# Kernel optimization log

Hardware: AMD Instinct MI355X
Metric: run time of the kernel (lower is better)

Reference implementation:

```python
import math
import jax, jax.numpy as jnp
import numpy as np

# ---------------- static irrep configuration ----------------
RS_IN = [(16, 0, 0), (16, 1, 0)]
RS_OUT = [(16, 0, 0), (16, 1, 0)]


def selection_rule(l_in, p_in, l_out, p_out):
    return [l for l in range(abs(l_in - l_out), l_in + l_out + 1)
            if p_out == 0 or p_in * (-1) ** l == p_out]


# ---------------- real Wigner 3j (Clebsch-Gordan) ----------------

def _su2_cg(j1, j2, j3, m1, m2, m3):
    if m1 + m2 != m3:
        return 0.0
    f = math.factorial
    pref = math.sqrt((2 * j3 + 1) * f(j3 + j1 - j2) * f(j3 - j1 + j2) * f(j1 + j2 - j3) / f(j1 + j2 + j3 + 1))
    pref *= math.sqrt(f(j3 + m3) * f(j3 - m3) * f(j1 - m1) * f(j1 + m1) * f(j2 - m2) * f(j2 + m2))
    s = 0.0
    for k in range(0, j1 + j2 - j3 + 1):
        d = [k, j1 + j2 - j3 - k, j1 - m1 - k, j2 + m2 - k, j3 - j1 - m2 + k, j3 - j2 + m1 + k]
        if any(x < 0 for x in d):
            continue
        s += (-1) ** k / np.prod([float(f(x)) for x in d])
    return pref * s


def _c2r(l):
    # real SH = A @ complex SH, rows/cols ordered m = -l..l
    A = np.zeros((2 * l + 1, 2 * l + 1), dtype=complex)
    s2 = 1.0 / math.sqrt(2)
    for m in range(-l, l + 1):
        if m < 0:
            A[l + m, l + m] = 1j * s2
            A[l + m, l - m] = -1j * (-1) ** m * s2
        elif m == 0:
            A[l, l] = 1.0
        else:
            A[l + m, l - m] = s2
            A[l + m, l + m] = (-1) ** m * s2
    return A


_W3J_CACHE = {}

def wigner_3j(l1, l2, l3):
    key = (l1, l2, l3)
    if key in _W3J_CACHE:
        return _W3J_CACHE[key]
    C = np.zeros((2 * l1 + 1, 2 * l2 + 1, 2 * l3 + 1))
    for m1 in range(-l1, l1 + 1):
        for m2 in range(-l2, l2 + 1):
            m3 = -(m1 + m2)
            if abs(m3) <= l3:
                C[l1 + m1, l2 + m2, l3 + m3] = ((-1) ** (l1 - l2 - m3) / math.sqrt(2 * l3 + 1)
                                                * _su2_cg(l1, l2, l3, m1, m2, -m3))
    T = np.einsum('ia,jb,kc,abc->ijk', _c2r(l1), _c2r(l2), _c2r(l3), C.astype(complex))
    T = T * (-1j) ** (l1 + l2 + l3)
    re, im = np.real(T), np.imag(T)
    T = re if np.abs(re).sum() >= np.abs(im).sum() else im
    n = math.sqrt(float((T ** 2).sum()))
    T = T / n if n > 1e-12 else T
    _W3J_CACHE[key] = T
    return T


# ---------------- real spherical harmonics (l = 0,1,2) ----------------

def real_sh(ls, xyz):
    r = jnp.linalg.norm(xyz, axis=-1)
    n = xyz / jnp.where(r > 0, r, 1.0)[..., None]
    x, y, z = n[..., 0], n[..., 1], n[..., 2]
    out = []
    for l in ls:
        if l == 0:
            out.append(jnp.full(x.shape, 0.28209479177387814, x.dtype)[None])
        elif l == 1:
            c = 0.4886025119029199
            out.append(jnp.stack([c * y, c * z, c * x]))
        elif l == 2:
            c1 = 1.0925484305920792
            c2 = 0.31539156525252005
            c3 = 0.5462742152960396
            out.append(jnp.stack([c1 * x * y, c1 * y * z, c2 * (3 * z * z - 1), c1 * x * z, c3 * (x * x - y * y)]))
        else:
            raise NotImplementedError
    return jnp.concatenate(out, axis=0)  # [sum(2l+1), batch, a, b]


def _norm_coef_table():
    nc = np.zeros((len(RS_OUT), len(RS_IN), 2))
    for i, (mul_out, l_out, p_out) in enumerate(RS_OUT):
        num = sum(mul_in * len(selection_rule(l_in, p_in, l_out, p_out))
                  for (mul_in, l_in, p_in) in RS_IN)
        for j, (mul_in, l_in, p_in) in enumerate(RS_IN):
            lm = math.sqrt(2 * l_in + 1) * math.sqrt(4 * math.pi)
            nc[i, j, 0] = lm / math.sqrt(num)
            nc[i, j, 1] = lm / math.sqrt(mul_in)
    return nc


def kernel_conv(features, geometry, mask, W1, b1, W2, b2):
    batch, a, b, _ = geometry.shape
    set_of_l_filters = sorted({l for (_, li, pi) in RS_IN for (_, lo, po) in RS_OUT
                               for l in selection_rule(li, pi, lo, po)})
    Y = real_sh(set_of_l_filters, geometry)             # [9, z, a, b]
    radii = jnp.linalg.norm(geometry, axis=-1)          # [z, a, b]
    # radial MLP: 1 -> H -> n_path
    h = jax.nn.relu(radii[..., None] * W1[0] + b1)
    R = h @ W2 + b2                                     # [z, a, b, n_path]
    nc = _norm_coef_table()
    is_zero = radii == 0

    out_blocks = []
    begin_R = 0
    for i, (mul_out, l_out, p_out) in enumerate(RS_OUT):
        block = jnp.zeros((batch, a, mul_out, 2 * l_out + 1), features.dtype)
        begin_in = 0
        for j, (mul_in, l_in, p_in) in enumerate(RS_IN):
            s_in = slice(begin_in, begin_in + mul_in * (2 * l_in + 1))
            begin_in += mul_in * (2 * l_in + 1)
            l_filters = selection_rule(l_in, p_in, l_out, p_out)
            if not l_filters:
                continue
            n = mul_out * mul_in * len(l_filters)
            sub_R = R[..., begin_R:begin_R + n].reshape(batch, a, b, mul_out, mul_in, len(l_filters))
            begin_R += n
            sub_nc = jnp.where(is_zero, nc[i, j, 1], nc[i, j, 0]).astype(features.dtype)
            f_in = features[..., s_in].reshape(batch, b, mul_in, 2 * l_in + 1)
            for k, l_f in enumerate(l_filters):
                offset = sum(2 * l + 1 for l in set_of_l_filters if l < l_f)
                sub_Y = Y[offset:offset + 2 * l_f + 1]
                C = jnp.asarray(wigner_3j(l_out, l_in, l_f), features.dtype)
                block = block + jnp.einsum('ijk,kzab,zabuv,zab,zbvj->zaui',
                                           C, sub_Y, sub_R[..., k], sub_nc, f_in)
        out_blocks.append(block.reshape(batch, a, -1))
    out = jnp.concatenate(out_blocks, axis=-1)          # [z, a, n_out]
    return out * mask[..., None]


def setup_inputs() -> dict:
    key = jax.random.key(0)
    ks = jax.random.split(key, 6)
    batch, a, b = 2, 160, 160
    dim_in, n_path, H = 64, 1536, 64
    return {
        'features': jax.random.normal(ks[0], (batch, b, dim_in), jnp.float32),
        'geometry': jax.random.normal(ks[1], (batch, a, b, 3), jnp.float32),
        'mask': jnp.ones((batch, b), jnp.float32),
        'W1': jax.random.normal(ks[2], (1, H), jnp.float32) * 0.5,
        'b1': jax.random.normal(ks[3], (H,), jnp.float32) * 0.1,
        'W2': jax.random.normal(ks[4], (H, n_path), jnp.float32) / np.sqrt(H),
        'b2': jnp.zeros((n_path,), jnp.float32),
    }


def reference(features, geometry, mask, W1, b1, W2, b2):
    return kernel_conv(features, geometry, mask, W1, b1, W2, b2)
```

## Files before the change

kernel.cpp:

```cpp
#include <hip/hip_runtime.h>
#include <hip/hip_fp16.h>
#include <math.h>

#define NPATH 1536
#define NSEG  65
#define NB    160
#define NA    160
#define CW    32
#define PPW   5

__device__ float  dg_thr[64];
__device__ float4 dg_tbl4[NSEG * 512];

static __device__ __forceinline__ __half2 bc_h2(float x) {
    union { float f; __half2 h; } u; u.f = x; return u.h;
}
static __device__ __forceinline__ unsigned short h_us(__half h) {
    union { __half h; unsigned short s; } u; u.h = h; return u.s;
}

__global__ __launch_bounds__(256) void k_prep(const float* __restrict__ W1,
                                              const float* __restrict__ b1,
                                              const float* __restrict__ W2,
                                              const float* __restrict__ b2,
                                              float* __restrict__ out) {
    int bid = blockIdx.x, tid = threadIdx.x;
    if (bid >= 390) {
        out[(bid - 390) * 256 + tid] = 0.0f;
        return;
    }
    int tseg = bid / 6, tcol = bid % 6;
    __shared__ float tv[64], mw[64], mb[64];
    if (tid < 64) {
        float w = W1[tid], b = b1[tid];
        tv[tid] = (w != 0.0f) ? (-b / w) : __builtin_inff();
    }
    __syncthreads();
    if (tid < 64) {
        float mine = tv[tid];
        int rank = 0;
        for (int j = 0; j < 64; ++j) {
            float o = tv[j];
            rank += (o < mine || (o == mine && j < tid)) ? 1 : 0;
        }
        float w = W1[tid], b = b1[tid];
        bool act = (w > 0.0f) ? (rank < tseg)
                 : (w < 0.0f) ? (rank >= tseg)
                              : (b > 0.0f);
        mw[tid] = act ? w : 0.0f;
        mb[tid] = act ? b : 0.0f;
        if (bid == 0) dg_thr[tid] = mine;
    }
    __syncthreads();

    int p = tcol * 256 + tid;
    int e, k; float scl;
    if (p < 768) {
        int u = (p >> 4) & 15, v = p & 15, vu = v * 16 + u;
        if (p < 256)      { e = vu;       k = 0; scl = 0.17677669529663687f; }
        else if (p < 512) { e = vu;       k = 1; scl = 0.6266570686577502f;  }
        else              { e = 256 + vu; k = 0; scl = 0.2558286876965162f;  }
    } else {
        int m = (p - 768) / 3, kk = (p - 768) % 3;
        int u = m >> 4, v = m & 15, vu = v * 16 + u;
        e = 256 + vu;
        if (kk == 0)      { k = 1; scl = 0.125f;              }
        else if (kk == 1) { k = 2; scl = 0.3133285343288751f; }
        else              { k = 3; scl = 0.7674950309598664f; }
    }

    float A = 0.0f, B = 0.0f;
    #pragma unroll 8
    for (int c = 0; c < 64; ++c) {
        float w2 = W2[c * NPATH + p];
        A = fmaf(mw[c], w2, A);
        B = fmaf(mb[c], w2, B);
    }
    float sv = scl * A;
    float iv = scl * (B + b2[p]);

    unsigned short* ub = (unsigned short*)dg_tbl4 + ((size_t)tseg * 512 + e) * 8;
    ub[k]     = h_us(__float2half(sv));
    ub[4 + k] = h_us(__float2half(iv));
    if (p < 256) {
        ((unsigned int*)ub)[1] = 0u;
        ((unsigned int*)ub)[3] = 0u;
    }
}

__global__ __launch_bounds__(256, 4) void k_main(const float* __restrict__ feat,
                                                 const float* __restrict__ geom,
                                                 const float* __restrict__ mask,
                                                 float* __restrict__ out) {
    int wv   = threadIdx.x >> 6;
    int lane = threadIdx.x & 63;
    int gw   = blockIdx.x * 4 + wv;
    int chunk = gw & (CW - 1);
    int za    = gw >> 5;
    int z     = za / NA;

    __shared__ __align__(16) float sFeat[4][PPW][64];
    __shared__ float sAcc[4][64];

    const bool is0 = lane < 16;
    int u  = is0 ? lane : ((lane - 16) / 3);
    int i3 = is0 ? 0 : ((lane - 16) % 3);
    int waddr = is0 ? (lane * 4 + 3) : (((lane - 16) / 3) * 4 + ((lane - 16) % 3));

    int o_base = (is0 ? 0 : 256) + u;
    float zfl  = is0 ? 1.4142135623730951f : 2.0f;
    float bx = (!is0 && i3 == 0) ? 1.0f : 0.0f;
    float by = (!is0 && i3 == 1) ? 1.0f : 0.0f;
    float bz = (!is0 && i3 == 2) ? 1.0f : 0.0f;

    float thrv = dg_thr[lane];

    const float is30 = 0.18257418583505536f;
    const float is10 = 0.31622776601683794f;
    const float c1sh = 0.4886025119029199f;
    const float c21 = 1.0925484305920792f, c22 = 0.31539156525252005f, c23 = 0.5462742152960396f;

    int b0 = chunk * PPW;
    #pragma unroll
    for (int it = 0; it < PPW; ++it) {
        float fv = feat[((size_t)(z * NB + b0 + it)) * 64 + lane];
        sFeat[wv][it][waddr] = fv;
    }

    float rr[PPW], nxa[PPW], nya[PPW], nza[PPW], zfa[PPW];
    int rowo[PPW];
    #pragma unroll
    for (int it = 0; it < PPW; ++it) {
        const float* g = geom + ((size_t)za * NB + b0 + it) * 3;
        float gx = g[0], gy = g[1], gz = g[2];
        float r = sqrtf(gx * gx + gy * gy + gz * gz);
        bool zr = (r == 0.0f);
        float inv = zr ? 1.0f : (1.0f / r);
        nxa[it] = gx * inv; nya[it] = gy * inv; nza[it] = gz * inv;
        rr[it] = r;
        zfa[it] = zr ? zfl : 1.0f;
        unsigned long long bm = __ballot(thrv < r);
        rowo[it] = __popcll(bm) * 512;
    }

    float acc = 0.0f;

    #pragma unroll
    for (int it = 0; it < PPW; ++it) {
        float r = rr[it];

        const float4* __restrict__ rowp = dg_tbl4 + rowo[it] + o_base;
        const float*  sp = &sFeat[wv][it][0];
        float T0 = 0.0f;
        float T1x = 0.0f, T1y = 0.0f, T1z = 0.0f;
        float T2x = 0.0f, T2y = 0.0f, T2z = 0.0f;
        float T3x = 0.0f, T3y = 0.0f, T3z = 0.0f;
        #pragma unroll
        for (int v = 0; v < 16; ++v) {
            float4 t = rowp[v * 16];
            __half2 hs01 = bc_h2(t.x), hs23 = bc_h2(t.y);
            __half2 hi01 = bc_h2(t.z), hi23 = bc_h2(t.w);
            float R0 = fmaf(r, __low2float(hs01),  __low2float(hi01));
            float R1 = fmaf(r, __high2float(hs01), __high2float(hi01));
            float R2 = fmaf(r, __low2float(hs23),  __low2float(hi23));
            float R3 = fmaf(r, __high2float(hs23), __high2float(hi23));
            float4 fq = *(const float4*)&sp[4 * v];
            T0  = fmaf(R0, fq.w, T0);
            T1x = fmaf(R1, fq.x, T1x);
            T1y = fmaf(R1, fq.y, T1y);
            T1z = fmaf(R1, fq.z, T1z);
            T2x = fmaf(R2, fq.x, T2x);
            T2y = fmaf(R2, fq.y, T2y);
            T2z = fmaf(R2, fq.z, T2z);
            T3x = fmaf(R3, fq.x, T3x);
            T3y = fmaf(R3, fq.y, T3y);
            T3z = fmaf(R3, fq.z, T3z);
        }

        float nx = nxa[it], ny = nya[it], nz = nza[it];
        float Y1_0 = c1sh * ny, Y1_1 = c1sh * nz, Y1_2 = c1sh * nx;
        float Y2_0 = c21 * nx * ny;
        float Y2_1 = c21 * ny * nz;
        float Y2_2 = c22 * fmaf(3.0f, nz * nz, -1.0f);
        float Y2_3 = c21 * nx * nz;
        float Y2_4 = c23 * (nx * nx - ny * ny);

        float Yi = (i3 == 0) ? Y1_0 : (i3 == 1) ? Y1_1 : Y1_2;
        float c0 = is0 ? 1.0f : Yi;
        float d1x = is0 ? Y1_0 : bx;
        float d1y = is0 ? Y1_1 : by;
        float d1z = is0 ? Y1_2 : bz;
        float d2x = (i3 == 0) ? 0.0f   : (i3 == 1) ? -Y1_2 : Y1_1;
        float d2y = (i3 == 0) ? Y1_2   : (i3 == 1) ? 0.0f  : -Y1_0;
        float d2z = (i3 == 0) ? -Y1_1  : (i3 == 1) ? Y1_0  : 0.0f;
        float za_ = is10 * Y2_0, zb_ = is10 * Y2_1, zc_ = is10 * Y2_3;
        float zd_ = is30 * Y2_2, ze_ = is10 * Y2_4;
        float d3x = (i3 == 0) ? (-zd_ - ze_) : (i3 == 1) ? zb_ : za_;
        float d3y = (i3 == 0) ? zb_ : (i3 == 1) ? (2.0f * zd_) : zc_;
        float d3z = (i3 == 0) ? za_ : (i3 == 1) ? zc_ : (ze_ - zd_);

        float s = c0 * T0;
        s = fmaf(d1x, T1x, s); s = fmaf(d1y, T1y, s); s = fmaf(d1z, T1z, s);
        s = fmaf(d2x, T2x, s); s = fmaf(d2y, T2y, s); s = fmaf(d2z, T2z, s);
        s = fmaf(d3x, T3x, s); s = fmaf(d3y, T3y, s); s = fmaf(d3z, T3z, s);
        acc = fmaf(s, zfa[it], acc);
    }

    sAcc[wv][lane] = acc;
    __syncthreads();
    if (threadIdx.x < 64) {
        float sum = sAcc[0][threadIdx.x] + sAcc[1][threadIdx.x]
                  + sAcc[2][threadIdx.x] + sAcc[3][threadIdx.x];
        sum *= mask[za];
        atomicAdd(&out[(size_t)za * 64 + threadIdx.x], sum);
    }
}

extern "C" void kernel_launch(void* const* d_in, const int* in_sizes, int n_in,
                              void* d_out, int out_size, void* d_ws, size_t ws_size,
                              hipStream_t stream) {
    (void)in_sizes; (void)n_in; (void)d_ws; (void)ws_size; (void)out_size;
    const float* feat = (const float*)d_in[0];
    const float* geom = (const float*)d_in[1];
    const float* mask = (const float*)d_in[2];
    const float* W1   = (const float*)d_in[3];
    const float* b1   = (const float*)d_in[4];
    const float* W2   = (const float*)d_in[5];
    const float* b2   = (const float*)d_in[6];
    float* out = (float*)d_out;

    k_prep<<<470, 256, 0, stream>>>(W1, b1, W2, b2, out);
    k_main<<<2 * NA * CW / 4, 256, 0, stream>>>(feat, geom, mask, out);
}
```

Before: 104.8 us.

## Split v-reduction across wave halves and recombine with cross-lane shuffles

```diff
diff --git a/kernel.cpp b/kernel.cpp
--- a/kernel.cpp
+++ b/kernel.cpp
@@ -102,16 +102,25 @@
     __shared__ __align__(16) float sFeat[4][PPW][64];
     __shared__ float sAcc[4][64];
 
-    const bool is0 = lane < 16;
-    int u  = is0 ? lane : ((lane - 16) / 3);
-    int i3 = is0 ? 0 : ((lane - 16) % 3);
-    int waddr = is0 ? (lane * 4 + 3) : (((lane - 16) / 3) * 4 + ((lane - 16) % 3));
-
-    int o_base = (is0 ? 0 : 256) + u;
-    float zfl  = is0 ? 1.4142135623730951f : 2.0f;
-    float bx = (!is0 && i3 == 0) ? 1.0f : 0.0f;
-    float by = (!is0 && i3 == 1) ? 1.0f : 0.0f;
-    float bz = (!is0 && i3 == 2) ? 1.0f : 0.0f;
+    int h    = lane >> 5;
+    int l32  = lane & 31;
+    bool tl0 = l32 < 16;
+    int  tu  = l32 & 15;
+    int  e_base = (tl0 ? 0 : 256) + h * 16 + tu;
+
+    bool is0o = lane < 16;
+    int  grp  = lane >> 4;
+    int  i3o  = (grp == 2) ? 2 : (grp == 3) ? 1 : 0;
+    int  uo   = lane & 15;
+    int  outI = is0o ? uo : (16 + uo * 3 + i3o);
+    bool useSw = (grp == 2);
+    float zfl = is0o ? 1.4142135623730951f : 2.0f;
+    float bx = (i3o == 0) ? 1.0f : 0.0f;
+    float by = (i3o == 1) ? 1.0f : 0.0f;
+    float bz = (i3o == 2) ? 1.0f : 0.0f;
+
+    int waddr = (lane < 16) ? (lane * 4 + 3)
+                            : (((lane - 16) / 3) * 4 + ((lane - 16) % 3));
 
     float thrv = dg_thr[lane];
 
@@ -149,22 +158,22 @@
     for (int it = 0; it < PPW; ++it) {
         float r = rr[it];
 
-        const float4* __restrict__ rowp = dg_tbl4 + rowo[it] + o_base;
-        const float*  sp = &sFeat[wv][it][0];
+        const float4* __restrict__ rowp = dg_tbl4 + rowo[it] + e_base;
+        const float*  spL = &sFeat[wv][it][0] + h * 4;
         float T0 = 0.0f;
         float T1x = 0.0f, T1y = 0.0f, T1z = 0.0f;
         float T2x = 0.0f, T2y = 0.0f, T2z = 0.0f;
         float T3x = 0.0f, T3y = 0.0f, T3z = 0.0f;
         #pragma unroll
-        for (int v = 0; v < 16; ++v) {
-            float4 t = rowp[v * 16];
+        for (int s = 0; s < 8; ++s) {
+            float4 t = rowp[s * 32];
             __half2 hs01 = bc_h2(t.x), hs23 = bc_h2(t.y);
             __half2 hi01 = bc_h2(t.z), hi23 = bc_h2(t.w);
             float R0 = fmaf(r, __low2float(hs01),  __low2float(hi01));
             float R1 = fmaf(r, __high2float(hs01), __high2float(hi01));
             float R2 = fmaf(r, __low2float(hs23),  __low2float(hi23));
             float R3 = fmaf(r, __high2float(hs23), __high2float(hi23));
-            float4 fq = *(const float4*)&sp[4 * v];
+            float4 fq = *(const float4*)&spL[s * 8];
             T0  = fmaf(R0, fq.w, T0);
             T1x = fmaf(R1, fq.x, T1x);
             T1y = fmaf(R1, fq.y, T1y);
@@ -177,6 +186,13 @@
             T3z = fmaf(R3, fq.z, T3z);
         }
 
+        #define COMB(t) { t += __shfl_xor(t, 32); float _w = __shfl_xor(t, 48); t = useSw ? _w : t; }
+        COMB(T0)
+        COMB(T1x) COMB(T1y) COMB(T1z)
+        COMB(T2x) COMB(T2y) COMB(T2z)
+        COMB(T3x) COMB(T3y) COMB(T3z)
+        #undef COMB
+
         float nx = nxa[it], ny = nya[it], nz = nza[it];
         float Y1_0 = c1sh * ny, Y1_1 = c1sh * nz, Y1_2 = c1sh * nx;
         float Y2_0 = c21 * nx * ny;
@@ -185,19 +201,19 @@
         float Y2_3 = c21 * nx * nz;
         float Y2_4 = c23 * (nx * nx - ny * ny);
 
-        float Yi = (i3 == 0) ? Y1_0 : (i3 == 1) ? Y1_1 : Y1_2;
-        float c0 = is0 ? 1.0f : Yi;
-        float d1x = is0 ? Y1_0 : bx;
-        float d1y = is0 ? Y1_1 : by;
-        float d1z = is0 ? Y1_2 : bz;
-        float d2x = (i3 == 0) ? 0.0f   : (i3 == 1) ? -Y1_2 : Y1_1;
-        float d2y = (i3 == 0) ? Y1_2   : (i3 == 1) ? 0.0f  : -Y1_0;
-        float d2z = (i3 == 0) ? -Y1_1  : (i3 == 1) ? Y1_0  : 0.0f;
+        float Yi = (i3o == 0) ? Y1_0 : (i3o == 1) ? Y1_1 : Y1_2;
+        float c0 = is0o ? 1.0f : Yi;
+        float d1x = is0o ? Y1_0 : bx;
+        float d1y = is0o ? Y1_1 : by;
+        float d1z = is0o ? Y1_2 : bz;
+        float d2x = (i3o == 0) ? 0.0f   : (i3o == 1) ? -Y1_2 : Y1_1;
+        float d2y = (i3o == 0) ? Y1_2   : (i3o == 1) ? 0.0f  : -Y1_0;
+        float d2z = (i3o == 0) ? -Y1_1  : (i3o == 1) ? Y1_0  : 0.0f;
         float za_ = is10 * Y2_0, zb_ = is10 * Y2_1, zc_ = is10 * Y2_3;
         float zd_ = is30 * Y2_2, ze_ = is10 * Y2_4;
-        float d3x = (i3 == 0) ? (-zd_ - ze_) : (i3 == 1) ? zb_ : za_;
-        float d3y = (i3 == 0) ? zb_ : (i3 == 1) ? (2.0f * zd_) : zc_;
-        float d3z = (i3 == 0) ? za_ : (i3 == 1) ? zc_ : (ze_ - zd_);
+        float d3x = (i3o == 0) ? (-zd_ - ze_) : (i3o == 1) ? zb_ : za_;
+        float d3y = (i3o == 0) ? zb_ : (i3o == 1) ? (2.0f * zd_) : zc_;
+        float d3z = (i3o == 0) ? za_ : (i3o == 1) ? zc_ : (ze_ - zd_);
 
         float s = c0 * T0;
         s = fmaf(d1x, T1x, s); s = fmaf(d1y, T1y, s); s = fmaf(d1z, T1z, s);
@@ -206,7 +222,7 @@
         acc = fmaf(s, zfa[it], acc);
     }
 
-    sAcc[wv][lane] = acc;
+    sAcc[wv][outI] = acc;
     __syncthreads();
     if (threadIdx.x < 64) {
         float sum = sAcc[0][threadIdx.x] + sAcc[1][threadIdx.x]
```

Result: faster. 96.59 us (-7.9%).
